# Kernel optimization log

Hardware: AMD Instinct MI355X
Metric: run time of the kernel (lower is better)

The kernel has to match this reference:

```python
import jax, jax.numpy as jnp
import numpy as np

N = 262144
E = 2097152
IMG = 120.0
VOX = 16.0
GRID = 8  # ceil(120/16)
NUM_GRIDS = GRID * GRID
EPS = 1e-5


def setup_inputs() -> dict:
    key = jax.random.key(0)
    ks = jax.random.split(key, 16)
    x = jax.random.normal(ks[0], (N, 1), dtype=jnp.float32)
    pos = jax.random.uniform(ks[1], (N, 3), dtype=jnp.float32) * IMG
    edge_index = jax.random.randint(ks[2], (2, E), 0, N, dtype=jnp.int64)
    # conv1: PointNetConv-style local linear on concat([x_j, pos_j - pos_i]) -> 16
    W1 = jax.random.normal(ks[3], (1 + 3, 16), dtype=jnp.float32) * 0.3
    b1 = jax.random.normal(ks[4], (16,), dtype=jnp.float32) * 0.05
    bn1_mean = jax.random.uniform(ks[5], (16,), dtype=jnp.float32)
    bn1_var = jax.random.uniform(ks[6], (16,), dtype=jnp.float32)
    bn1_w = jax.random.uniform(ks[7], (16,), dtype=jnp.float32)
    bn1_b = jax.random.uniform(ks[8], (16,), dtype=jnp.float32)
    # conv2: 16 -> 32
    W2 = jax.random.normal(ks[9], (16 + 3, 32), dtype=jnp.float32) * 0.2
    b2 = jax.random.normal(ks[10], (32,), dtype=jnp.float32) * 0.05
    bn2_mean = jax.random.uniform(ks[11], (32,), dtype=jnp.float32)
    bn2_var = jax.random.uniform(ks[12], (32,), dtype=jnp.float32)
    bn2_w = jax.random.uniform(ks[13], (32,), dtype=jnp.float32)
    bn2_b = jax.random.uniform(ks[14], (32,), dtype=jnp.float32)
    return dict(x=x, pos=pos, edge_index=edge_index,
                W1=W1, b1=b1, bn1_mean=bn1_mean, bn1_var=bn1_var, bn1_w=bn1_w, bn1_b=bn1_b,
                W2=W2, b2=b2, bn2_mean=bn2_mean, bn2_var=bn2_var, bn2_w=bn2_w, bn2_b=bn2_b)


def _conv_bn_relu(x, pos, src, dst, W, b, mean, var, gamma, beta):
    # message: linear(concat([x_j, pos_j - pos_i])), max aggregation over incoming edges
    rel = pos[src] - pos[dst]                       # [E, 3]
    msg = jnp.concatenate([x[src], rel], axis=1) @ W + b  # [E, C_out]
    agg = jax.ops.segment_max(msg, dst, num_segments=N)   # [N, C_out]
    agg = jnp.where(jnp.isneginf(agg), 0.0, agg)    # nodes with no incoming edges -> 0
    # BatchNorm1d in eval mode (running stats) + ReLU
    y = (agg - mean) * jax.lax.rsqrt(var + EPS) * gamma + beta
    return jax.nn.relu(y)


def reference(x, pos, edge_index, W1, b1, bn1_mean, bn1_var, bn1_w, bn1_b,
              W2, b2, bn2_mean, bn2_var, bn2_w, bn2_b):
    src, dst = edge_index[0], edge_index[1]
    h1 = _conv_bn_relu(x, pos, src, dst, W1, b1, bn1_mean, bn1_var, bn1_w, bn1_b)
    h2 = _conv_bn_relu(h1, pos, src, dst, W2, b2, bn2_mean, bn2_var, bn2_w, bn2_b)
    # MaxPoolingX: voxel-grid cluster on pos[:, :2] with voxel size 16 over 120x120 -> 8x8 grid
    gx = jnp.floor(pos[:, 0] / VOX).astype(jnp.int32)
    gy = jnp.floor(pos[:, 1] / VOX).astype(jnp.int32)
    cluster = jnp.clip(gx + gy * GRID, 0, NUM_GRIDS - 1)
    pooled = jax.ops.segment_max(h2, cluster, num_segments=NUM_GRIDS)  # [64, 32]
    pooled = jnp.where(jnp.isneginf(pooled), 0.0, pooled)
    return pooled
```

## Files before the change

kernel.cpp:

```cpp
#include <hip/hip_runtime.h>
#include <hip/hip_fp16.h>

#define N_NODES 262144
#define N_EDGES 2097152
#define EPS_BN 1e-5f
#define NBUCK 1024
#define BCAP 2560

__device__ __forceinline__ unsigned enc(float f) {
    unsigned u = __float_as_uint(f);
    return (u & 0x80000000u) ? ~u : (u | 0x80000000u);
}
__device__ __forceinline__ float dec(unsigned u) {
    unsigned b = (u & 0x80000000u) ? (u & 0x7FFFFFFFu) : ~u;
    return __uint_as_float(b);
}

__global__ __launch_bounds__(256) void part_k(const int* __restrict__ ei,
                                              int* __restrict__ bcur,
                                              unsigned* __restrict__ pairs2) {
    __shared__ int hh[NBUCK], bb[NBUCK];
    int t = threadIdx.x;
    for (int i = t; i < NBUCK; i += 256) hh[i] = 0;
    __syncthreads();
    int base = blockIdx.x * 4096;
    for (int k = 0; k < 16; ++k) {
        int d = ei[N_EDGES + base + k * 256 + t];
        atomicAdd(&hh[d >> 8], 1);
    }
    __syncthreads();
    for (int i = t; i < NBUCK; i += 256) {
        int c = hh[i];
        bb[i] = c ? atomicAdd(&bcur[i], c) : 0;
        hh[i] = 0;
    }
    __syncthreads();
    for (int k = 0; k < 16; ++k) {
        int e = base + k * 256 + t;
        int d = ei[N_EDGES + e], s = ei[e];
        int b = d >> 8;
        int r = atomicAdd(&hh[b], 1);
        int slot = bb[b] + r;
        if (slot < BCAP)
            pairs2[(size_t)b * BCAP + slot] = (unsigned)s | ((unsigned)(d & 255) << 18);
    }
}

__global__ __launch_bounds__(256) void pack_px(const float* __restrict__ pos,
                                               const float* __restrict__ x,
                                               float4* __restrict__ px4) {
    int i = blockIdx.x * 256 + threadIdx.x;
    px4[i] = make_float4(pos[3*i], pos[3*i+1], pos[3*i+2], x[i]);
}

__global__ __launch_bounds__(256) void conv1_push(
    const float4* __restrict__ px4, const float* __restrict__ pos,
    const unsigned* __restrict__ pairs2, const int* __restrict__ bcur,
    const float* __restrict__ W1, const float* __restrict__ b1,
    const float* __restrict__ mean, const float* __restrict__ var,
    const float* __restrict__ gamma, const float* __restrict__ beta_bn,
    const float* __restrict__ W2, const float* __restrict__ b2,
    __half* __restrict__ beta)
{
    __shared__ unsigned agg[256 * 16];
    for (int i = threadIdx.x; i < 256 * 16; i += 256) agg[i] = 0u;
    int b = blockIdx.x;
    int cnt = min(bcur[b], BCAP);
    const unsigned* P = pairs2 + (size_t)b * BCAP;
    int g = threadIdx.x >> 4, ch = threadIdx.x & 15;
    float w1xc = W1[ch], wrx = W1[16 + ch], wry = W1[32 + ch], wrz = W1[48 + ch];
    float b1c = b1[ch];
    __syncthreads();

    int e = g;
    for (; e + 48 < cnt; e += 64) {
        unsigned p0 = P[e], p1 = P[e+16], p2 = P[e+32], p3 = P[e+48];
        float4 q0 = px4[p0 & 0x3FFFFu];
        float4 q1 = px4[p1 & 0x3FFFFu];
        float4 q2 = px4[p2 & 0x3FFFFu];
        float4 q3 = px4[p3 & 0x3FFFFu];
        float a0 = b1c + w1xc*q0.w + wrx*q0.x + wry*q0.y + wrz*q0.z;
        float a1 = b1c + w1xc*q1.w + wrx*q1.x + wry*q1.y + wrz*q1.z;
        float a2 = b1c + w1xc*q2.w + wrx*q2.x + wry*q2.y + wrz*q2.z;
        float a3 = b1c + w1xc*q3.w + wrx*q3.x + wry*q3.y + wrz*q3.z;
        atomicMax(&agg[(p0 >> 18) * 16 + ch], enc(a0));
        atomicMax(&agg[(p1 >> 18) * 16 + ch], enc(a1));
        atomicMax(&agg[(p2 >> 18) * 16 + ch], enc(a2));
        atomicMax(&agg[(p3 >> 18) * 16 + ch], enc(a3));
    }
    for (; e < cnt; e += 16) {
        unsigned p = P[e];
        float4 q = px4[p & 0x3FFFFu];
        float a = b1c + w1xc*q.w + wrx*q.x + wry*q.y + wrz*q.z;
        atomicMax(&agg[(p >> 18) * 16 + ch], enc(a));
    }
    __syncthreads();

    float sc1 = gamma[ch] * rsqrtf(var[ch] + EPS_BN);
    float sh1 = beta_bn[ch] - mean[ch] * sc1;
    int dbase = b * 256;
    for (int slot = threadIdx.x; slot < 4096; slot += 256) {
        int d = slot >> 4, n = dbase + d;
        unsigned u = agg[slot];
        float px = pos[3*n], py = pos[3*n+1], pz = pos[3*n+2];
        float v = u ? (dec(u) - (wrx*px + wry*py + wrz*pz)) : 0.0f;
        ((float*)agg)[slot] = fmaxf(v * sc1 + sh1, 0.0f);
    }
    __syncthreads();

    int c = threadIdx.x & 31, row = threadIdx.x >> 5;
    float wc[16];
#pragma unroll
    for (int q = 0; q < 16; ++q) wc[q] = W2[q * 32 + c];
    float wxc = W2[512 + c], wyc = W2[544 + c], wzc = W2[576 + c], bc = b2[c];
    for (int d = row; d < 256; d += 8) {
        const float* h = (const float*)agg + d * 16;
        float bv = bc;
#pragma unroll
        for (int q = 0; q < 16; ++q) bv += wc[q] * h[q];
        int n = dbase + d;
        bv += wxc * pos[3*n] + wyc * pos[3*n+1] + wzc * pos[3*n+2];
        beta[(size_t)n * 32 + c] = __float2half(bv);
    }
}

__global__ __launch_bounds__(256) void conv2_push(
    const __half* __restrict__ beta, const float* __restrict__ pos,
    const unsigned* __restrict__ pairs2, const int* __restrict__ bcur,
    const float* __restrict__ W2,
    const float* __restrict__ mean, const float* __restrict__ var,
    const float* __restrict__ gamma, const float* __restrict__ beta_bn,
    unsigned* __restrict__ pool)
{
    __shared__ unsigned agg[256 * 32];
    __shared__ unsigned lpool[2048];
    for (int i = threadIdx.x; i < 256 * 32; i += 256) agg[i] = 0u;
    for (int i = threadIdx.x; i < 2048; i += 256) lpool[i] = 0u;
    int b = blockIdx.x;
    int cnt = min(bcur[b], BCAP);
    const unsigned* P = pairs2 + (size_t)b * BCAP;
    int g = threadIdx.x >> 5, ch = threadIdx.x & 31;
    float wrx = W2[512 + ch], wry = W2[544 + ch], wrz = W2[576 + ch];
    float sc = gamma[ch] * rsqrtf(var[ch] + EPS_BN);
    float sh = beta_bn[ch] - mean[ch] * sc;
    __syncthreads();

    int e = g;
    for (; e + 24 < cnt; e += 32) {
        unsigned p0 = P[e], p1 = P[e+8], p2 = P[e+16], p3 = P[e+24];
        float a0 = __half2float(beta[(size_t)(p0 & 0x3FFFFu) * 32 + ch]);
        float a1 = __half2float(beta[(size_t)(p1 & 0x3FFFFu) * 32 + ch]);
        float a2 = __half2float(beta[(size_t)(p2 & 0x3FFFFu) * 32 + ch]);
        float a3 = __half2float(beta[(size_t)(p3 & 0x3FFFFu) * 32 + ch]);
        atomicMax(&agg[(p0 >> 18) * 32 + ch], enc(a0));
        atomicMax(&agg[(p1 >> 18) * 32 + ch], enc(a1));
        atomicMax(&agg[(p2 >> 18) * 32 + ch], enc(a2));
        atomicMax(&agg[(p3 >> 18) * 32 + ch], enc(a3));
    }
    for (; e < cnt; e += 8) {
        unsigned p = P[e];
        float a = __half2float(beta[(size_t)(p & 0x3FFFFu) * 32 + ch]);
        atomicMax(&agg[(p >> 18) * 32 + ch], enc(a));
    }
    __syncthreads();

    int dbase = b * 256;
    for (int slot = threadIdx.x; slot < 8192; slot += 256) {
        int d = slot >> 5, n = dbase + d;
        unsigned u = agg[slot];
        float px = pos[3*n], py = pos[3*n+1], pz = pos[3*n+2];
        float v = u ? (dec(u) - (wrx*px + wry*py + wrz*pz)) : 0.0f;
        float y = fmaxf(v * sc + sh, 0.0f);
        int gx = (int)floorf(px * (1.0f/16.0f));
        int gy = (int)floorf(py * (1.0f/16.0f));
        int cl = min(max(gx + gy * 8, 0), 63);
        atomicMax(&lpool[cl * 32 + ch], enc(y));
    }
    __syncthreads();
    for (int i = threadIdx.x; i < 2048; i += 256) {
        unsigned u = lpool[i];
        if (u > pool[i]) atomicMax(&pool[i], u);
    }
}

__global__ __launch_bounds__(256) void pool_decode(const unsigned* __restrict__ pool,
                                                   float* __restrict__ out) {
    int i = blockIdx.x * 256 + threadIdx.x;
    unsigned u = pool[i];
    out[i] = (u == 0u) ? 0.0f : dec(u);
}

extern "C" void kernel_launch(void* const* d_in, const int* in_sizes, int n_in,
                              void* d_out, int out_size, void* d_ws, size_t ws_size,
                              hipStream_t stream) {
    const float* x    = (const float*)d_in[0];
    const float* pos  = (const float*)d_in[1];
    const int*   ei   = (const int*)d_in[2];
    const float* W1   = (const float*)d_in[3];
    const float* b1   = (const float*)d_in[4];
    const float* bn1m = (const float*)d_in[5];
    const float* bn1v = (const float*)d_in[6];
    const float* bn1w = (const float*)d_in[7];
    const float* bn1b = (const float*)d_in[8];
    const float* W2   = (const float*)d_in[9];
    const float* b2   = (const float*)d_in[10];
    const float* bn2m = (const float*)d_in[11];
    const float* bn2v = (const float*)d_in[12];
    const float* bn2w = (const float*)d_in[13];
    const float* bn2b = (const float*)d_in[14];

    size_t N = N_NODES;
    unsigned* pool   = (unsigned*)d_ws;
    int* bcur        = (int*)(pool + 2048);
    unsigned* pairs2 = (unsigned*)(bcur + NBUCK);
    float* px4       = (float*)(pairs2 + (size_t)NBUCK * BCAP);
    __half* beta     = (__half*)(px4 + 4 * N);

    hipMemsetAsync(d_ws, 0, (size_t)(2048 + NBUCK) * 4, stream);

    part_k      <<<N_EDGES/4096, 256, 0, stream>>>(ei, bcur, pairs2);
    pack_px     <<<N_NODES/256, 256, 0, stream>>>(pos, x, (float4*)px4);
    conv1_push  <<<NBUCK, 256, 0, stream>>>((const float4*)px4, pos, pairs2, bcur,
                                            W1, b1, bn1m, bn1v, bn1w, bn1b, W2, b2, beta);
    conv2_push  <<<NBUCK, 256, 0, stream>>>(beta, pos, pairs2, bcur,
                                            W2, bn2m, bn2v, bn2w, bn2b, pool);
    pool_decode <<<8, 256, 0, stream>>>(pool, (float*)d_out);
}
```

Measured before the change: 265.1 us.

## Fuse node packing into partition kernel and deepen conv2 gather unroll

Folds the pack_px kernel into part_k, so one launch both partitions the edges and packs pos/x into float4. The partition grid shrinks from 512 to 256 blocks, with each block handling twice as many edges. conv2_push now issues 8 independent gathers per iteration instead of 4 and sets a minimum-occupancy launch bound. The intent is to cut one launch and raise memory-level parallelism in the gather. The cost is fewer blocks for partitioning, more per-block atomics and register pressure in conv2.

```diff
diff --git a/kernel.cpp b/kernel.cpp
--- a/kernel.cpp
+++ b/kernel.cpp
@@ -6,6 +6,7 @@
 #define EPS_BN 1e-5f
 #define NBUCK 1024
 #define BCAP 2560
+#define PARTB 256
 
 __device__ __forceinline__ unsigned enc(float f) {
     unsigned u = __float_as_uint(f);
@@ -18,13 +19,16 @@
 
 __global__ __launch_bounds__(256) void part_k(const int* __restrict__ ei,
                                               int* __restrict__ bcur,
-                                              unsigned* __restrict__ pairs2) {
+                                              unsigned* __restrict__ pairs2,
+                                              const float* __restrict__ pos,
+                                              const float* __restrict__ x,
+                                              float4* __restrict__ px4) {
     __shared__ int hh[NBUCK], bb[NBUCK];
     int t = threadIdx.x;
     for (int i = t; i < NBUCK; i += 256) hh[i] = 0;
     __syncthreads();
-    int base = blockIdx.x * 4096;
-    for (int k = 0; k < 16; ++k) {
+    int base = blockIdx.x * (N_EDGES / PARTB);
+    for (int k = 0; k < N_EDGES / PARTB / 256; ++k) {
         int d = ei[N_EDGES + base + k * 256 + t];
         atomicAdd(&hh[d >> 8], 1);
     }
@@ -35,7 +39,7 @@
         hh[i] = 0;
     }
     __syncthreads();
-    for (int k = 0; k < 16; ++k) {
+    for (int k = 0; k < N_EDGES / PARTB / 256; ++k) {
         int e = base + k * 256 + t;
         int d = ei[N_EDGES + e], s = ei[e];
         int b = d >> 8;
@@ -44,13 +48,11 @@
         if (slot < BCAP)
             pairs2[(size_t)b * BCAP + slot] = (unsigned)s | ((unsigned)(d & 255) << 18);
     }
-}
-
-__global__ __launch_bounds__(256) void pack_px(const float* __restrict__ pos,
-                                               const float* __restrict__ x,
-                                               float4* __restrict__ px4) {
-    int i = blockIdx.x * 256 + threadIdx.x;
-    px4[i] = make_float4(pos[3*i], pos[3*i+1], pos[3*i+2], x[i]);
+    int nb = blockIdx.x * (N_NODES / PARTB);
+    for (int i = t; i < N_NODES / PARTB; i += 256) {
+        int n = nb + i;
+        px4[n] = make_float4(pos[3*n], pos[3*n+1], pos[3*n+2], x[n]);
+    }
 }
 
 __global__ __launch_bounds__(256) void conv1_push(
@@ -124,7 +126,7 @@
     }
 }
 
-__global__ __launch_bounds__(256) void conv2_push(
+__global__ __launch_bounds__(256, 6) void conv2_push(
     const __half* __restrict__ beta, const float* __restrict__ pos,
     const unsigned* __restrict__ pairs2, const int* __restrict__ bcur,
     const float* __restrict__ W2,
@@ -146,16 +148,17 @@
     __syncthreads();
 
     int e = g;
-    for (; e + 24 < cnt; e += 32) {
-        unsigned p0 = P[e], p1 = P[e+8], p2 = P[e+16], p3 = P[e+24];
-        float a0 = __half2float(beta[(size_t)(p0 & 0x3FFFFu) * 32 + ch]);
-        float a1 = __half2float(beta[(size_t)(p1 & 0x3FFFFu) * 32 + ch]);
-        float a2 = __half2float(beta[(size_t)(p2 & 0x3FFFFu) * 32 + ch]);
-        float a3 = __half2float(beta[(size_t)(p3 & 0x3FFFFu) * 32 + ch]);
-        atomicMax(&agg[(p0 >> 18) * 32 + ch], enc(a0));
-        atomicMax(&agg[(p1 >> 18) * 32 + ch], enc(a1));
-        atomicMax(&agg[(p2 >> 18) * 32 + ch], enc(a2));
-        atomicMax(&agg[(p3 >> 18) * 32 + ch], enc(a3));
+    for (; e + 56 < cnt; e += 64) {
+        unsigned p[8];
+        float a[8];
+#pragma unroll
+        for (int q = 0; q < 8; ++q) p[q] = P[e + q * 8];
+#pragma unroll
+        for (int q = 0; q < 8; ++q)
+            a[q] = __half2float(beta[(size_t)(p[q] & 0x3FFFFu) * 32 + ch]);
+#pragma unroll
+        for (int q = 0; q < 8; ++q)
+            atomicMax(&agg[(p[q] >> 18) * 32 + ch], enc(a[q]));
     }
     for (; e < cnt; e += 8) {
         unsigned p = P[e];
@@ -218,8 +221,7 @@
 
     hipMemsetAsync(d_ws, 0, (size_t)(2048 + NBUCK) * 4, stream);
 
-    part_k      <<<N_EDGES/4096, 256, 0, stream>>>(ei, bcur, pairs2);
-    pack_px     <<<N_NODES/256, 256, 0, stream>>>(pos, x, (float4*)px4);
+    part_k      <<<PARTB, 256, 0, stream>>>(ei, bcur, pairs2, pos, x, (float4*)px4);
     conv1_push  <<<NBUCK, 256, 0, stream>>>((const float4*)px4, pos, pairs2, bcur,
                                             W1, b1, bn1m, bn1v, bn1w, bn1b, W2, b2, beta);
     conv2_push  <<<NBUCK, 256, 0, stream>>>(beta, pos, pairs2, bcur,
```

Result: faster. 252.7 us (-4.7%).
